# Kernel tuning notes

Measured on AMD Instinct MI355X. Metric: run time of the kernel, lower is better.

Reference implementation:

```python
import jax, jax.numpy as jnp
import numpy as np


def setup_inputs() -> dict:
    key = jax.random.key(0)
    B, L = 32, 512
    k1, k2, k3, k4 = jax.random.split(key, 4)
    acids = jax.random.normal(k1, (B, L), dtype=jnp.float32)
    mask = jnp.ones((B, L), dtype=jnp.float32)
    # Self-avoiding-style lattice walk: unit step along a random axis each move.
    axis = jax.random.randint(k3, (B, L - 1), 0, 3)
    sign = jax.random.randint(k4, (B, L - 1), 0, 2) * 2 - 1
    steps = (jax.nn.one_hot(axis, 3, dtype=jnp.int32) * sign[..., None]).astype(jnp.int32)
    idx = jnp.concatenate([jnp.zeros((B, 1, 3), jnp.int32), jnp.cumsum(steps, axis=1)], axis=1)
    idx = jnp.clip(idx, -(L - 1), L - 1)  # keep coords in the op's valid range
    return {"acids": acids, "mask": mask, "idx": idx, "protein_length": 512, "window_size": 9}


def reference(acids, mask, idx, protein_length, window_size):
    # acids: [B, L] float, mask: [B, L] float, idx: [B, L, 3] int lattice coords.
    L, W = protein_length, window_size
    B = acids.shape[0]
    W3 = W * W * W
    half = W // 2

    # Map walk coords [-(L-1), L-1] -> even grid coords [0, 4(L-1)].
    idx2 = 2 * (idx + (L - 1))                          # [B, L, 3] int32, all even
    # AVG pool window [2] stride 1 VALID on even ints -> exact integer midpoints.
    inter_idx = (idx2[:, :-1, :] + idx2[:, 1:, :]) // 2  # [B, L-1, 3] odd coords
    # 2 * avgpool(acids) + 1 == acids[i] + acids[i+1] + 1
    inter_vals = acids[:, :-1] + acids[:, 1:] + 1.0      # [B, L-1]

    cidx = jnp.concatenate([idx2, inter_idx], axis=1)    # [B, M, 3], M = 2L-1
    cval = jnp.concatenate([acids, inter_vals], axis=1)  # [B, M]
    cmask = jnp.concatenate([mask, mask[:, 1:]], axis=1) # [B, M]

    # Per residue i: a W^3 window centered at idx2[:, i]. Scatter every snake
    # point (residues + bond midpoints) that falls inside the window.
    rel = cidx[:, None, :, :] - idx2[:, :, None, :] + half     # [B, L, M, 3]
    valid = jnp.all((rel >= 0) & (rel < W), axis=-1)           # [B, L, M]
    lin = (rel[..., 0] * W + rel[..., 1]) * W + rel[..., 2]    # [B, L, M]
    lin = jnp.where(valid, lin, 0)
    val = jnp.where(valid, (cval * cmask)[:, None, :], 0.0)    # [B, L, M]

    b_off = jnp.arange(B, dtype=jnp.int32)[:, None, None] * (L * W3)
    i_off = jnp.arange(L, dtype=jnp.int32)[None, :, None] * W3
    g = (b_off + i_off + lin).reshape(-1)
    lattice = jnp.zeros((B * L * W3,), dtype=acids.dtype).at[g].add(val.reshape(-1))
    return lattice.reshape(B, L, W, W, W, 1)
```

## Files before the change

kernel.cpp:

```cpp
#include <hip/hip_runtime.h>
#include <hip/hip_bf16.h>


constexpr int L  = 512;
constexpr int W  = 9;
constexpr int W3 = W * W * W;
constexpr int HALF = W / 2;
constexpr int M  = 2 * L - 1;

__global__ __launch_bounds__(256) void lattice_snake_kernel(
    const float* __restrict__ acids,
    const float* __restrict__ mask,
    const int*   __restrict__ idx,
    float*       __restrict__ out)
{
    const int bi = blockIdx.x;
    const int b  = bi >> 9;
    const int i  = bi & (L - 1);

    __shared__ float win[W3];
    for (int k = threadIdx.x; k < W3; k += blockDim.x) win[k] = 0.0f;
    __syncthreads();

    const int*   idxb = idx   + (size_t)b * L * 3;
    const float* ab   = acids + (size_t)b * L;
    const float* mb   = mask  + (size_t)b * L;

    const int cx = 2 * idxb[3 * i + 0] + 2 * (L - 1);
    const int cy = 2 * idxb[3 * i + 1] + 2 * (L - 1);
    const int cz = 2 * idxb[3 * i + 2] + 2 * (L - 1);

    for (int m = threadIdx.x; m < M; m += blockDim.x) {
        int px, py, pz;
        float v;
        if (m < L) {
            px = 2 * idxb[3 * m + 0] + 2 * (L - 1);
            py = 2 * idxb[3 * m + 1] + 2 * (L - 1);
            pz = 2 * idxb[3 * m + 2] + 2 * (L - 1);
            v  = ab[m] * mb[m];
        } else {
            const int j = m - L;
            px = idxb[3 * j + 0] + idxb[3 * j + 3] + 2 * (L - 1);
            py = idxb[3 * j + 1] + idxb[3 * j + 4] + 2 * (L - 1);
            pz = idxb[3 * j + 2] + idxb[3 * j + 5] + 2 * (L - 1);
            v  = (ab[j] + ab[j + 1] + 1.0f) * mb[j + 1];
        }
        const int rx = px - cx + HALF;
        const int ry = py - cy + HALF;
        const int rz = pz - cz + HALF;
        if ((unsigned)rx < (unsigned)W && (unsigned)ry < (unsigned)W &&
            (unsigned)rz < (unsigned)W) {
            atomicAdd(&win[(rx * W + ry) * W + rz], v);
        }
    }
    __syncthreads();

    float* ob = out + (size_t)bi * W3;
    for (int k = threadIdx.x; k < W3; k += blockDim.x) ob[k] = win[k];
}

extern "C" void kernel_launch(void* const* d_in, const int* in_sizes, int n_in,
                              void* d_out, int out_size, void* d_ws, size_t ws_size,
                              hipStream_t stream) {
    const float* acids = (const float*)d_in[0];
    const float* mask  = (const float*)d_in[1];
    const int*   idx   = (const int*)d_in[2];
    float*       out   = (float*)d_out;

    const int B = in_sizes[0] / L;
    const int nblocks = B * L;

    lattice_snake_kernel<<<nblocks, 256, 0, stream>>>(acids, mask, idx, out);
}
```

Baseline: 96.12 us.

## Share one bounding-box scatter across groups of eight consecutive residue windows

Each block now handles 8 consecutive residues. It scatters all snake points once into a shared-memory bounding box covering the union of their windows, then extracts each 9^3 window from that box, with non-temporal stores to the output. This cuts the redundant scan of all 1023 points per residue by a factor of 8. In exchange each block does more serial extraction work, there are 8x fewer blocks, and shared memory grows to a 23^3 box. Because consecutive lattice coordinates differ by unit steps, the box stays within bounds.

```diff
diff --git a/kernel.cpp b/kernel.cpp
--- a/kernel.cpp
+++ b/kernel.cpp
@@ -2,11 +2,14 @@
 #include <hip/hip_bf16.h>
 
 
-constexpr int L  = 512;
-constexpr int W  = 9;
-constexpr int W3 = W * W * W;
+constexpr int L    = 512;
+constexpr int W    = 9;
+constexpr int W3   = W * W * W;
 constexpr int HALF = W / 2;
-constexpr int M  = 2 * L - 1;
+constexpr int M    = 2 * L - 1;
+constexpr int G    = 8;
+constexpr int BOXW = 2 * (G - 1) + W;
+constexpr int BOXN = BOXW * BOXW * BOXW;
 
 __global__ __launch_bounds__(256) void lattice_snake_kernel(
     const float* __restrict__ acids,
@@ -14,23 +17,41 @@
     const int*   __restrict__ idx,
     float*       __restrict__ out)
 {
-    const int bi = blockIdx.x;
-    const int b  = bi >> 9;
-    const int i  = bi & (L - 1);
-
-    __shared__ float win[W3];
-    for (int k = threadIdx.x; k < W3; k += blockDim.x) win[k] = 0.0f;
-    __syncthreads();
+    const int blk = blockIdx.x;
+    const int b   = blk >> 6;
+    const int g   = blk & 63;
+    const int i0  = g * G;
+    const int tid = threadIdx.x;
 
     const int*   idxb = idx   + (size_t)b * L * 3;
     const float* ab   = acids + (size_t)b * L;
     const float* mb   = mask  + (size_t)b * L;
 
-    const int cx = 2 * idxb[3 * i + 0] + 2 * (L - 1);
-    const int cy = 2 * idxb[3 * i + 1] + 2 * (L - 1);
-    const int cz = 2 * idxb[3 * i + 2] + 2 * (L - 1);
+    int cxs[G], cys[G], czs[G];
+    int mnx =  1 << 30, mny =  1 << 30, mnz =  1 << 30;
+    int mxx = -(1 << 30), mxy = -(1 << 30), mxz = -(1 << 30);
+#pragma unroll
+    for (int w = 0; w < G; ++w) {
+        const int ii = i0 + w;
+        const int cx = 2 * idxb[3 * ii + 0] + 2 * (L - 1);
+        const int cy = 2 * idxb[3 * ii + 1] + 2 * (L - 1);
+        const int cz = 2 * idxb[3 * ii + 2] + 2 * (L - 1);
+        cxs[w] = cx; cys[w] = cy; czs[w] = cz;
+        mnx = min(mnx, cx); mxx = max(mxx, cx);
+        mny = min(mny, cy); mxy = max(mxy, cy);
+        mnz = min(mnz, cz); mxz = max(mxz, cz);
+    }
+    const int ox = mnx - HALF, oy = mny - HALF, oz = mnz - HALF;
+    const int dxd = mxx - mnx + W;
+    const int dyd = mxy - mny + W;
+    const int dzd = mxz - mnz + W;
+    const int nbox = dxd * dyd * dzd;
 
-    for (int m = threadIdx.x; m < M; m += blockDim.x) {
+    __shared__ float box[BOXN];
+    for (int k = tid; k < nbox; k += 256) box[k] = 0.0f;
+    __syncthreads();
+
+    for (int m = tid; m < M; m += 256) {
         int px, py, pz;
         float v;
         if (m < L) {
@@ -45,18 +66,30 @@
             pz = idxb[3 * j + 2] + idxb[3 * j + 5] + 2 * (L - 1);
             v  = (ab[j] + ab[j + 1] + 1.0f) * mb[j + 1];
         }
-        const int rx = px - cx + HALF;
-        const int ry = py - cy + HALF;
-        const int rz = pz - cz + HALF;
-        if ((unsigned)rx < (unsigned)W && (unsigned)ry < (unsigned)W &&
-            (unsigned)rz < (unsigned)W) {
-            atomicAdd(&win[(rx * W + ry) * W + rz], v);
+        const int rx = px - ox, ry = py - oy, rz = pz - oz;
+        if ((unsigned)rx < (unsigned)dxd && (unsigned)ry < (unsigned)dyd &&
+            (unsigned)rz < (unsigned)dzd) {
+            atomicAdd(&box[(rx * dyd + ry) * dzd + rz], v);
         }
     }
     __syncthreads();
 
-    float* ob = out + (size_t)bi * W3;
-    for (int k = threadIdx.x; k < W3; k += blockDim.x) ob[k] = win[k];
+    float* ob = out + ((size_t)b * L + i0) * W3;
+#pragma unroll
+    for (int w = 0; w < G; ++w) {
+        const int bx = cxs[w] - HALF - ox;
+        const int by = cys[w] - HALF - oy;
+        const int bz = czs[w] - HALF - oz;
+        for (int k = tid; k < W3; k += 256) {
+            const int dx = k / 81;
+            const int r  = k - dx * 81;
+            const int dy = r / 9;
+            const int dz = r - dy * 9;
+            const float val =
+                box[((bx + dx) * dyd + (by + dy)) * dzd + (bz + dz)];
+            __builtin_nontemporal_store(val, &ob[(size_t)w * W3 + k]);
+        }
+    }
 }
 
 extern "C" void kernel_launch(void* const* d_in, const int* in_sizes, int n_in,
@@ -68,7 +101,7 @@
     float*       out   = (float*)d_out;
 
     const int B = in_sizes[0] / L;
-    const int nblocks = B * L;
+    const int nblocks = B * (L / G);
 
     lattice_snake_kernel<<<nblocks, 256, 0, stream>>>(acids, mask, idx, out);
 }
```

New measurement: 88.27 us. 1.09x faster.
